# Optimization experiments

Hardware: AMD Instinct MI355X
Metric: run time of the kernel (lower is better)

The kernel has to match this reference:

```python
import jax, jax.numpy as jnp
import numpy as np

N = 100_000       # nodes
E = 1_600_000     # edges (avg degree 16)
IN_DIM = 256
OUT_DIM = 64
NEG_SLOPE = 0.01  # F.leaky_relu default


def setup_inputs() -> dict:
    key = jax.random.key(0)
    k1, k2, k3, k4, k5 = jax.random.split(key, 5)
    h = jax.random.normal(k1, (N, IN_DIM), jnp.float32)
    fc_w = jax.random.normal(k2, (IN_DIM, OUT_DIM), jnp.float32) / np.sqrt(IN_DIM)
    attn_w = jax.random.normal(k3, (2 * OUT_DIM,), jnp.float32) / np.sqrt(2 * OUT_DIM)
    src = jax.random.randint(k4, (E,), 0, N, jnp.int32)
    dst = jax.random.randint(k5, (E,), 0, N, jnp.int32)
    return {"h": h, "fc_w": fc_w, "attn_w": attn_w, "src": src, "dst": dst}


def reference(h, fc_w, attn_w, src, dst):
    # z = fc(h)
    z = h @ fc_w                                    # [N, D]
    # attn_fc(cat(z_src, z_dst)) == z_src @ a_l + z_dst @ a_r
    s_src = z @ attn_w[:OUT_DIM]                    # [N]
    s_dst = z @ attn_w[OUT_DIM:]                    # [N]
    e = jax.nn.leaky_relu(s_src[src] + s_dst[dst], NEG_SLOPE)  # [E]
    # per-destination segment softmax (stable)
    e_max = jax.ops.segment_max(e, dst, num_segments=N)        # [N]
    e_max = jnp.where(jnp.isfinite(e_max), e_max, 0.0)         # nodes w/o in-edges
    ex = jnp.exp(e - e_max[dst])                               # [E]
    denom = jax.ops.segment_sum(ex, dst, num_segments=N)       # [N]
    alpha = ex / jnp.maximum(denom[dst], 1e-9)                 # [E]
    # weighted scatter-sum of source features
    h_out = jax.ops.segment_sum(alpha[:, None] * z[src], dst, num_segments=N)  # [N, D]
    return h_out
```

## Files before the change

kernel.cpp:

```cpp
#include <hip/hip_runtime.h>
#include <hip/hip_bf16.h>
#include <math.h>

#define IN_DIM 256
#define OUT_DIM 64
#define NEG_SLOPE 0.01f
#define NBSHIFT 7
#define BNODES 128
#define BCAP 2560
#define A_CHUNK 4096

typedef __attribute__((ext_vector_type(8))) short short8;
typedef __attribute__((ext_vector_type(4))) float f32x4;

__device__ __forceinline__ unsigned short f2bf_rne(float f) {
    unsigned u = __builtin_bit_cast(unsigned, f);
    u += 0x7FFF + ((u >> 16) & 1);
    return (unsigned short)(u >> 16);
}
__device__ __forceinline__ float bflo(unsigned v) {
    return __builtin_bit_cast(float, v << 16);
}
__device__ __forceinline__ float bfhi(unsigned v) {
    return __builtin_bit_cast(float, v & 0xFFFF0000u);
}
__device__ __forceinline__ unsigned cvtpk_bf16(float lo, float hi) {
    unsigned r;
    asm("v_cvt_pk_bf16_f32 %0, %1, %2" : "=v"(r) : "v"(lo), "v"(hi));
    return r;
}

__global__ __launch_bounds__(256) void k_prep(
    const float* __restrict__ fcw, unsigned short* __restrict__ bhi,
    int* __restrict__ gcnt, int NB)
{
    int t = blockIdx.x * 256 + threadIdx.x;
    if (t < NB) gcnt[t] = 0;
    if (t >= 2048) return;
    int lane = t & 63;
    int nt = (t >> 6) & 3;
    int step = t >> 8;
    int kbase = step * 32 + (lane >> 4) * 8;
    int col = nt * 16 + (lane & 15);
#pragma unroll
    for (int i = 0; i < 8; ++i)
        bhi[t * 8 + i] = f2bf_rne(fcw[(size_t)(kbase + i) * OUT_DIM + col]);
}

__global__ __launch_bounds__(256, 4) void k_gemm(
    const float* __restrict__ h, const unsigned short* __restrict__ bhi,
    const float* __restrict__ attnw, unsigned short* __restrict__ zb,
    float* __restrict__ ssrc, float* __restrict__ sdst, int nrows)
{
    __shared__ short8 Bs[2048];
    const int tid = threadIdx.x;
    const int lane = tid & 63;
    const int wid = tid >> 6;
    const int rowbase = blockIdx.x * 64 + wid * 16;
    const int arow = rowbase + (lane & 15);
    const size_t abase = (size_t)min(arow, nrows - 1) * IN_DIM + (lane >> 4) * 8;

    float4 a[16];
#pragma unroll
    for (int s = 0; s < 8; ++s) {
        a[2 * s]     = *(const float4*)&h[abase + s * 32];
        a[2 * s + 1] = *(const float4*)&h[abase + s * 32 + 4];
    }
    asm volatile("" ::: "memory");

    short8 breg[8];
#pragma unroll
    for (int c = 0; c < 8; ++c)
        breg[c] = *(const short8*)&bhi[(c * 256 + tid) * 8];
#pragma unroll
    for (int c = 0; c < 8; ++c)
        Bs[c * 256 + tid] = breg[c];
    __syncthreads();

    short8 abf[8];
#pragma unroll
    for (int step = 0; step < 8; ++step) {
        uint4 pk;
        pk.x = cvtpk_bf16(a[2 * step].x,     a[2 * step].y);
        pk.y = cvtpk_bf16(a[2 * step].z,     a[2 * step].w);
        pk.z = cvtpk_bf16(a[2 * step + 1].x, a[2 * step + 1].y);
        pk.w = cvtpk_bf16(a[2 * step + 1].z, a[2 * step + 1].w);
        abf[step] = __builtin_bit_cast(short8, pk);
    }

    f32x4 acc[4] = {};
#pragma unroll
    for (int step = 0; step < 8; ++step) {
#pragma unroll
        for (int nt = 0; nt < 4; ++nt) {
            short8 bh = Bs[(step * 4 + nt) * 64 + lane];
            acc[nt] = __builtin_amdgcn_mfma_f32_16x16x32_bf16(
                abf[step], bh, acc[nt], 0, 0, 0);
        }
    }

    const int col = lane & 15;
    float aw1[4], aw2[4];
#pragma unroll
    for (int nt = 0; nt < 4; ++nt) {
        aw1[nt] = attnw[nt * 16 + col];
        aw2[nt] = attnw[OUT_DIM + nt * 16 + col];
    }
#pragma unroll
    for (int r = 0; r < 4; ++r) {
        int grow = rowbase + (lane >> 4) * 4 + r;
        float ss = 0.f, sd = 0.f;
#pragma unroll
        for (int nt = 0; nt < 4; ++nt) {
            float v = acc[nt][r];
            ss = fmaf(v, aw1[nt], ss);
            sd = fmaf(v, aw2[nt], sd);
            if (grow < nrows)
                zb[(size_t)grow * OUT_DIM + nt * 16 + col] = f2bf_rne(v);
        }
#pragma unroll
        for (int m = 8; m; m >>= 1) {
            ss += __shfl_xor(ss, m);
            sd += __shfl_xor(sd, m);
        }
        if (col == 0 && grow < nrows) { ssrc[grow] = ss; sdst[grow] = sd; }
    }
}

__global__ __launch_bounds__(256) void k_bin(
    const int* __restrict__ src, const int* __restrict__ dst,
    int* __restrict__ gcnt, int* __restrict__ gbuf, int E, int NB)
{
    __shared__ int cnt[1024];
    __shared__ int base[1024];
    int t = threadIdx.x;
    for (int i = t; i < NB; i += 256) cnt[i] = 0;
    __syncthreads();
    int ebase = blockIdx.x * A_CHUNK;
    int bkt[16], pkd[16];
#pragma unroll
    for (int i = 0; i < 16; ++i) {
        int e = ebase + t + i * 256;
        bkt[i] = -1;
        if (e < E) {
            int d = dst[e];
            int b = ((unsigned)d) >> NBSHIFT;
            bkt[i] = b;
            pkd[i] = ((d & (BNODES - 1)) << 24) | src[e];
            atomicAdd(&cnt[b], 1);
        }
    }
    __syncthreads();
    for (int i = t; i < NB; i += 256) {
        int c = cnt[i];
        base[i] = c ? (i * BCAP + atomicAdd(&gcnt[i], c)) : 0;
    }
    __syncthreads();
#pragma unroll
    for (int i = 0; i < 16; ++i) {
        if (bkt[i] >= 0) {
            int r = atomicAdd(&base[bkt[i]], 1);
            gbuf[r] = pkd[i];
        }
    }
}

__global__ __launch_bounds__(256) void k_aggr(
    const int* __restrict__ gcnt, const int* __restrict__ gbuf,
    const float* __restrict__ ssrc, const float* __restrict__ sdst,
    const unsigned short* __restrict__ zb, float* __restrict__ out, int N)
{
    __shared__ float2 pairs[BCAP];
    __shared__ int   ldeg[BNODES];
    __shared__ int   cur[BNODES];
    __shared__ float lsd[BNODES];
    __shared__ int2  se[BNODES];
    const int t = threadIdx.x;
    const int b = blockIdx.x;
    const int eb = b * BCAP;
    const int cnt = min(gcnt[b], BCAP);

    if (t < BNODES) {
        int node0 = (b << NBSHIFT) + t;
        ldeg[t] = 0;
        lsd[t] = (node0 < N) ? sdst[node0] : 0.f;
    }
    __syncthreads();
    for (int i = t; i < cnt; i += 256)
        atomicAdd(&ldeg[((unsigned)gbuf[eb + i]) >> 24], 1);
    __syncthreads();
    int own = (t < BNODES) ? ldeg[t] : 0;
    for (int o = 1; o < BNODES; o <<= 1) {
        int x = 0;
        if (t < BNODES && t >= o) x = ldeg[t - o];
        __syncthreads();
        if (t < BNODES && t >= o) ldeg[t] += x;
        __syncthreads();
    }
    if (t < BNODES) {
        int excl = ldeg[t] - own;
        cur[t] = excl;
        se[t] = make_int2(excl, excl + own);
    }
    __syncthreads();

    for (int cb = 0; cb < cnt; cb += 4096) {
        const int nloc = min(4096, cnt - cb);
        int p[16]; float w[16];
#pragma unroll
        for (int k = 0; k < 16; ++k) {
            int i = t + k * 256;
            if (i < nloc) {
                p[k] = gbuf[eb + cb + i];
                float x = ssrc[p[k] & 0xFFFFFF] + lsd[((unsigned)p[k]) >> 24];
                x = (x > 0.f) ? x : NEG_SLOPE * x;
                w[k] = __expf(x);
            }
        }
#pragma unroll
        for (int k = 0; k < 16; ++k) {
            int i = t + k * 256;
            if (i < nloc) {
                int r = atomicAdd(&cur[((unsigned)p[k]) >> 24], 1);
                pairs[r] = make_float2(
                    w[k], __builtin_bit_cast(float, (p[k] & 0xFFFFFF) << 7));
            }
        }
    }
    __syncthreads();

    const int g = t >> 4;
    const int li8 = (t & 15) * 8;
#pragma unroll
    for (int j = 0; j < BNODES / 16; ++j) {
        const int ln = g * (BNODES / 16) + j;
        const int node = (b << NBSHIFT) + ln;
        if (node >= N) continue;
        const int2 s = se[ln];
        float denom = 0.f, a0 = 0.f, a1 = 0.f, a2 = 0.f, a3 = 0.f;
#pragma unroll 4
        for (int i = s.x; i < s.y; ++i) {
            float2 pw = pairs[i];
            const float w = pw.x;
            const int off = __builtin_bit_cast(int, pw.y) + li8;
            const uint2 v = *(const uint2*)((const char*)zb + off);
            a0 = fmaf(w, bflo(v.x), a0);
            a1 = fmaf(w, bfhi(v.x), a1);
            a2 = fmaf(w, bflo(v.y), a2);
            a3 = fmaf(w, bfhi(v.y), a3);
            denom += w;
        }
        const float inv = 1.f / fmaxf(denom, 1e-9f);
        *(float4*)&out[(size_t)node * OUT_DIM + (t & 15) * 4] =
            make_float4(a0 * inv, a1 * inv, a2 * inv, a3 * inv);
    }
}

extern "C" void kernel_launch(void* const* d_in, const int* in_sizes, int n_in,
                              void* d_out, int out_size, void* d_ws, size_t ws_size,
                              hipStream_t stream)
{
    const float* h     = (const float*)d_in[0];
    const float* fcw   = (const float*)d_in[1];
    const float* attnw = (const float*)d_in[2];
    const int*   src   = (const int*)d_in[3];
    const int*   dst   = (const int*)d_in[4];
    const int N = in_sizes[0] / IN_DIM;
    const int E = in_sizes[3];
    float* out = (float*)d_out;

    const int NB = (N + BNODES - 1) >> NBSHIFT;
    const int NWGA = (E + A_CHUNK - 1) / A_CHUNK;

    char* ws = (char*)d_ws;
    size_t off = 0;
    auto carve = [&](size_t bytes) -> void* {
        void* p = ws + off;
        off = (off + bytes + 255) & ~(size_t)255;
        return p;
    };
    unsigned short* zb = (unsigned short*)carve((size_t)N * OUT_DIM * 2);
    float* ssrc     = (float*)carve((size_t)N * 4);
    float* sdst     = (float*)carve((size_t)N * 4);
    int*   gbuf     = (int*)carve((size_t)NB * BCAP * 4);
    unsigned short* bhi = (unsigned short*)carve(2048 * 8 * 2);
    int* gcnt  = (int*)carve((size_t)NB * 4);

    k_prep<<<8, 256, 0, stream>>>(fcw, bhi, gcnt, NB);
    k_gemm<<<(N + 63) / 64, 256, 0, stream>>>(h, bhi, attnw, zb, ssrc, sdst, N);
    k_bin<<<NWGA, 256, 0, stream>>>(src, dst, gcnt, gbuf, E, NB);
    k_aggr<<<NB, 256, 0, stream>>>(gcnt, gbuf, ssrc, sdst, zb, out, N);
}
```

Baseline: 102.0 us.

## Fuse edge binning into GEMM kernel via interleaved block roles

Merges the independent GEMM and edge-binning kernels into one launch, where every f-th block performs binning and the rest compute the projection GEMM. This removes one kernel launch and its tail/drain gap, and lets the memory-bound binning overlap with the GEMM blocks. The cost is higher shared memory per block (Bs plus cnt/base arrays), which may lower occupancy for the GEMM blocks.

New measurement: 111.2 us. +9.0%, slower.

```diff
diff --git a/kernel.cpp b/kernel.cpp
--- a/kernel.cpp
+++ b/kernel.cpp
@@ -47,16 +47,59 @@
         bhi[t * 8 + i] = f2bf_rne(fcw[(size_t)(kbase + i) * OUT_DIM + col]);
 }
 
-__global__ __launch_bounds__(256, 4) void k_gemm(
+__global__ __launch_bounds__(256, 4) void k_fused(
     const float* __restrict__ h, const unsigned short* __restrict__ bhi,
     const float* __restrict__ attnw, unsigned short* __restrict__ zb,
-    float* __restrict__ ssrc, float* __restrict__ sdst, int nrows)
+    float* __restrict__ ssrc, float* __restrict__ sdst, int nrows,
+    const int* __restrict__ src, const int* __restrict__ dst,
+    int* __restrict__ gcnt, int* __restrict__ gbuf, int E, int NB,
+    int nbin, int f)
 {
     __shared__ short8 Bs[2048];
-    const int tid = threadIdx.x;
-    const int lane = tid & 63;
-    const int wid = tid >> 6;
-    const int rowbase = blockIdx.x * 64 + wid * 16;
+    __shared__ int cnt[1024];
+    __shared__ int base[1024];
+
+    const int bid = blockIdx.x;
+    const int t = threadIdx.x;
+    const bool isbin = ((bid % f) == 0) && ((bid / f) < nbin);
+
+    if (isbin) {
+        for (int i = t; i < NB; i += 256) cnt[i] = 0;
+        __syncthreads();
+        const int ebase = (bid / f) * A_CHUNK;
+        int bkt[16], pkd[16];
+#pragma unroll
+        for (int i = 0; i < 16; ++i) {
+            int e = ebase + t + i * 256;
+            bkt[i] = -1;
+            if (e < E) {
+                int d = dst[e];
+                int b = ((unsigned)d) >> NBSHIFT;
+                bkt[i] = b;
+                pkd[i] = ((d & (BNODES - 1)) << 24) | src[e];
+                atomicAdd(&cnt[b], 1);
+            }
+        }
+        __syncthreads();
+        for (int i = t; i < NB; i += 256) {
+            int c = cnt[i];
+            base[i] = c ? (i * BCAP + atomicAdd(&gcnt[i], c)) : 0;
+        }
+        __syncthreads();
+#pragma unroll
+        for (int i = 0; i < 16; ++i) {
+            if (bkt[i] >= 0) {
+                int r = atomicAdd(&base[bkt[i]], 1);
+                gbuf[r] = pkd[i];
+            }
+        }
+        return;
+    }
+
+    const int gemmid = bid - min(bid / f + ((bid % f) ? 1 : 0), nbin);
+    const int lane = t & 63;
+    const int wid = t >> 6;
+    const int rowbase = gemmid * 64 + wid * 16;
     const int arow = rowbase + (lane & 15);
     const size_t abase = (size_t)min(arow, nrows - 1) * IN_DIM + (lane >> 4) * 8;
 
@@ -71,10 +114,10 @@
     short8 breg[8];
 #pragma unroll
     for (int c = 0; c < 8; ++c)
-        breg[c] = *(const short8*)&bhi[(c * 256 + tid) * 8];
+        breg[c] = *(const short8*)&bhi[(c * 256 + t) * 8];
 #pragma unroll
     for (int c = 0; c < 8; ++c)
-        Bs[c * 256 + tid] = breg[c];
+        Bs[c * 256 + t] = breg[c];
     __syncthreads();
 
     short8 abf[8];
@@ -124,44 +167,6 @@
             sd += __shfl_xor(sd, m);
         }
         if (col == 0 && grow < nrows) { ssrc[grow] = ss; sdst[grow] = sd; }
-    }
-}
-
-__global__ __launch_bounds__(256) void k_bin(
-    const int* __restrict__ src, const int* __restrict__ dst,
-    int* __restrict__ gcnt, int* __restrict__ gbuf, int E, int NB)
-{
-    __shared__ int cnt[1024];
-    __shared__ int base[1024];
-    int t = threadIdx.x;
-    for (int i = t; i < NB; i += 256) cnt[i] = 0;
-    __syncthreads();
-    int ebase = blockIdx.x * A_CHUNK;
-    int bkt[16], pkd[16];
-#pragma unroll
-    for (int i = 0; i < 16; ++i) {
-        int e = ebase + t + i * 256;
-        bkt[i] = -1;
-        if (e < E) {
-            int d = dst[e];
-            int b = ((unsigned)d) >> NBSHIFT;
-            bkt[i] = b;
-            pkd[i] = ((d & (BNODES - 1)) << 24) | src[e];
-            atomicAdd(&cnt[b], 1);
-        }
-    }
-    __syncthreads();
-    for (int i = t; i < NB; i += 256) {
-        int c = cnt[i];
-        base[i] = c ? (i * BCAP + atomicAdd(&gcnt[i], c)) : 0;
-    }
-    __syncthreads();
-#pragma unroll
-    for (int i = 0; i < 16; ++i) {
-        if (bkt[i] >= 0) {
-            int r = atomicAdd(&base[bkt[i]], 1);
-            gbuf[r] = pkd[i];
-        }
     }
 }
 
@@ -270,7 +275,10 @@
     float* out = (float*)d_out;
 
     const int NB = (N + BNODES - 1) >> NBSHIFT;
-    const int NWGA = (E + A_CHUNK - 1) / A_CHUNK;
+    const int nbin = (E + A_CHUNK - 1) / A_CHUNK;
+    const int ngemm = (N + 63) / 64;
+    const int grid = ngemm + nbin;
+    const int f = grid / nbin;
 
     char* ws = (char*)d_ws;
     size_t off = 0;
@@ -287,7 +295,7 @@
     int* gcnt  = (int*)carve((size_t)NB * 4);
 
     k_prep<<<8, 256, 0, stream>>>(fcw, bhi, gcnt, NB);
-    k_gemm<<<(N + 63) / 64, 256, 0, stream>>>(h, bhi, attnw, zb, ssrc, sdst, N);
-    k_bin<<<NWGA, 256, 0, stream>>>(src, dst, gcnt, gbuf, E, NB);
+    k_fused<<<grid, 256, 0, stream>>>(h, bhi, attnw, zb, ssrc, sdst, N,
+                                      src, dst, gcnt, gbuf, E, NB, nbin, f);
     k_aggr<<<NB, 256, 0, stream>>>(gcnt, gbuf, ssrc, sdst, zb, out, N);
 }
```
